# Kernel tuning notes

Measured on AMD Instinct MI355X. Metric: run time of the kernel, lower is better.

The kernel has to match this reference:

```python
import jax, jax.numpy as jnp
import numpy as np

N = 30000       # num atoms (all examples concatenated)
E = 480000      # total num edges (avg degree 16)
H = 128         # hidden_channels
R = 50          # num_rbf
NB = 3          # num interaction blocks
NEX = 64        # num examples (molecules)
NTYPES = 100    # atom type vocabulary
CUT = 10.0      # cutoff_upper


def setup_inputs() -> dict:
    key = jax.random.key(0)
    ks = jax.random.split(key, 20)
    s = 0.05
    inp = {
        "pos": jax.random.uniform(ks[0], (N, 3), dtype=jnp.float32) * 10.0,
        "atom_types": jax.random.randint(ks[1], (N,), 0, NTYPES),
        "edge_index": jax.random.randint(ks[2], (2, E), 0, N),
        "batch": jnp.sort(jax.random.randint(ks[3], (N,), 0, NEX)),
        # learned parameters
        "embedding": jax.random.normal(ks[4], (NTYPES, H), dtype=jnp.float32) * s,
        "filt_w1": jax.random.normal(ks[5], (NB, R, H), dtype=jnp.float32) * s,
        "filt_b1": jnp.zeros((NB, H), jnp.float32),
        "filt_w2": jax.random.normal(ks[6], (NB, H, H), dtype=jnp.float32) * s,
        "filt_b2": jnp.zeros((NB, H), jnp.float32),
        "lin1_w": jax.random.normal(ks[7], (NB, H, H), dtype=jnp.float32) * s,  # no bias
        "lin2_w": jax.random.normal(ks[8], (NB, H, H), dtype=jnp.float32) * s,
        "lin2_b": jnp.zeros((NB, H), jnp.float32),
        "blk_w": jax.random.normal(ks[9], (NB, H, H), dtype=jnp.float32) * s,
        "blk_b": jnp.zeros((NB, H), jnp.float32),
        "out_w1": jax.random.normal(ks[10], (H, H // 2), dtype=jnp.float32) * s,
        "out_b1": jnp.zeros((H // 2,), jnp.float32),
        "out_w2": jax.random.normal(ks[11], (H // 2, 1), dtype=jnp.float32) * s,
        "out_b2": jnp.zeros((1,), jnp.float32),
    }
    return inp


def reference(pos, atom_types, edge_index, batch, embedding,
              filt_w1, filt_b1, filt_w2, filt_b2,
              lin1_w, lin2_w, lin2_b, blk_w, blk_b,
              out_w1, out_b1, out_w2, out_b2):
    src, dst = edge_index[0], edge_index[1]
    # pairwise distances along edges
    diff = pos[src] - pos[dst]                        # [E,3]
    d = jnp.sqrt(jnp.sum(diff * diff, axis=-1) + 1e-12)  # [E]
    # Gaussian RBF expansion (PyG GaussianSmearing)
    offset = jnp.linspace(0.0, CUT, R, dtype=jnp.float32)
    coeff = -0.5 / (offset[1] - offset[0]) ** 2
    rbf = jnp.exp(coeff * (d[:, None] - offset) ** 2)  # [E,R]
    # cosine cutoff envelope
    C = 0.5 * (jnp.cos(d * jnp.pi / CUT) + 1.0) * (d < CUT)  # [E]

    x = embedding[atom_types]                         # [N,H]
    for b in range(NB):
        # filter network: Linear -> Tanh -> Linear, modulated by cutoff
        W = jnp.tanh(rbf @ filt_w1[b] + filt_b1[b]) @ filt_w2[b] + filt_b2[b]
        W = W * C[:, None]                            # [E,H]
        # cfconv: lin1 (no bias), gather-multiply-scatter, lin2
        h = x @ lin1_w[b]                             # [N,H]
        msg = h[src] * W                              # [E,H]
        agg = jax.ops.segment_sum(msg, dst, num_segments=N)  # [N,H]
        h = agg @ lin2_w[b] + lin2_b[b]
        # interaction block: activation + linear, residual update
        x = x + (jnp.tanh(h) @ blk_w[b] + blk_b[b])
    # output network: per-atom energy then scatter-sum per molecule
    e = jnp.tanh(x @ out_w1 + out_b1) @ out_w2 + out_b2     # [N,1]
    energy = jax.ops.segment_sum(e, batch, num_segments=NEX)  # [NEX,1]
    return energy.reshape(-1)
```

## Files before the change

kernel.cpp:

```cpp
#include <hip/hip_runtime.h>

typedef unsigned short ushort_t;
typedef _Float16 half8 __attribute__((ext_vector_type(8)));
typedef float f32x4 __attribute__((ext_vector_type(4)));

constexpr int NN  = 30000;
constexpr int EE  = 480000;
constexpr int NEXM = 64;
constexpr int ATB = 16;
constexpr int NSB = (NN + 255) / 256;
constexpr int NBINS = 2048;
constexpr int TROWS = 2064;

#define MFMA16(a,b,c) __builtin_amdgcn_mfma_f32_16x16x32_f16((a),(b),(c),0,0,0)
#define LDS_ADD(p,v) __hip_atomic_fetch_add((p),(v),__ATOMIC_RELAXED,__HIP_MEMORY_SCOPE_WORKGROUP)
#define LGKM_WAIT asm volatile("s_waitcnt lgkmcnt(0)" ::: "memory")

__device__ __forceinline__ float fast_tanh(float x){
  float e2 = __builtin_amdgcn_exp2f(x * 2.885390081777927f);
  return 1.f - 2.f * __builtin_amdgcn_rcpf(e2 + 1.f);
}
__device__ __forceinline__ ushort_t f2h(float v){
  union { _Float16 h; ushort_t s; } cv; cv.h = (_Float16)v; return cv.s;
}

__global__ __launch_bounds__(256) void prep_weights(
  const float* __restrict__ fw1, const float* __restrict__ fb1,
  const float* __restrict__ fw2, const float* __restrict__ l1w,
  const float* __restrict__ l2w, const float* __restrict__ bw,
  const float* __restrict__ ow1, ushort_t* __restrict__ frags)
{
  int u = blockIdx.x*256 + threadIdx.x;
  float val;
  if (u < 24576){
    int b = u >> 13; int v = u & 8191;
    int j = v & 7, lane = (v>>3)&63, fid = v>>9;
    int mt = fid>>1, ks = fid&1;
    int f1 = mt*16 + (lane&15);
    int k  = ks*32 + ((lane>>4)&3)*8 + j;
    val = (k < 50) ? fw1[(b*50 + k)*128 + f1] : (k == 50 ? fb1[b*128 + f1] : 0.f);
  } else if (u < 73728){
    int v = u - 24576; int b = v >> 14; int v2 = v & 16383;
    int j = v2&7, lane = (v2>>3)&63, fid = v2>>9;
    int mt = fid>>2, ks = fid&3;
    int n = mt*16 + (lane&15);
    int k = ks*32 + ((lane>>4)&3)*8 + j;
    val = fw2[b*16384 + k*128 + n];
  } else if (u < 221184){
    int v = u - 73728; int g = v / 49152; int v1 = v - g*49152;
    int b = v1 >> 14; int v2 = v1 & 16383;
    int j = v2&7, lane=(v2>>3)&63, fid=v2>>9;
    int mt = fid>>2, ks = fid&3;
    int n = mt*16 + (lane&15);
    int k = ks*32 + ((lane>>4)&3)*8 + j;
    const float* W = (g==0? l2w : (g==1? bw : l1w));
    val = W[b*16384 + k*128 + n];
  } else {
    int v2 = u - 221184;
    int j = v2&7, lane=(v2>>3)&63, fid=v2>>9;
    int mt = fid>>2, ks = fid&3;
    int n = mt*16 + (lane&15);
    int k = ks*32 + ((lane>>4)&3)*8 + j;
    val = ow1[k*64 + n];
  }
  frags[u] = f2h(val);
}

__global__ __launch_bounds__(256) void count_k(
  const int* __restrict__ ei, int* __restrict__ cnt)
{
  int e = blockIdx.x*256 + threadIdx.x;
  atomicAdd(cnt + ei[EE + e], 1);
}

__global__ __launch_bounds__(256) void scan1(
  const int* __restrict__ cnt, int* __restrict__ seg, int* __restrict__ bsum)
{
  __shared__ int ws[4];
  int i = blockIdx.x*256 + threadIdx.x;
  int lane = threadIdx.x & 63, w = threadIdx.x >> 6;
  int v = (i < NN) ? cnt[i] : 0;
  int s = v;
  #pragma unroll
  for (int o=1;o<64;o<<=1){ int t = __shfl_up(s,o,64); if (lane>=o) s += t; }
  if (lane == 63) ws[w] = s;
  __syncthreads();
  int add = 0;
  #pragma unroll
  for (int j=0;j<3;j++) if (w > j) add += ws[j];
  s += add;
  if (i < NN) seg[i] = s - v;
  if (threadIdx.x == 255) bsum[blockIdx.x] = s;
}

__global__ __launch_bounds__(128) void scan2(int* __restrict__ bsum)
{
  __shared__ int w0tot;
  int tid = threadIdx.x, lane = tid & 63, w = tid >> 6;
  int v = (tid < NSB) ? bsum[tid] : 0;
  int s = v;
  #pragma unroll
  for (int o=1;o<64;o<<=1){ int t = __shfl_up(s,o,64); if (lane>=o) s += t; }
  if (w == 0 && lane == 63) w0tot = s;
  __syncthreads();
  if (w == 1) s += w0tot;
  if (tid < NSB) bsum[tid] = s - v;
}

__global__ __launch_bounds__(256) void scan3(
  int* __restrict__ seg, const int* __restrict__ bsum)
{
  int i = blockIdx.x*256 + threadIdx.x;
  if (i < NN) seg[i] += bsum[blockIdx.x];
}

__global__ __launch_bounds__(256) void scatter_meta(
  const float* __restrict__ pos, const int* __restrict__ ei,
  int* __restrict__ off, uint2* __restrict__ meta2)
{
  int e = blockIdx.x*256 + threadIdx.x;
  int s = ei[e], d = ei[EE + e];
  float dx = pos[s*3+0]-pos[d*3+0];
  float dy = pos[s*3+1]-pos[d*3+1];
  float dz = pos[s*3+2]-pos[d*3+2];
  float dist = sqrtf(dx*dx+dy*dy+dz*dz + 1e-12f);
  float t = fminf(dist, 10.f) * ((float)NBINS / 10.f);
  int p = atomicAdd(off + d, 1);
  uint2 m;
  m.x = __float_as_uint(t);
  m.y = (unsigned)s;
  meta2[p] = m;
}

__global__ __launch_bounds__(256) void build_table(
  const ushort_t* __restrict__ w1a, const ushort_t* __restrict__ w2a,
  const float* __restrict__ fb2, ushort_t* __restrict__ tab)
{
  __shared__ ushort_t st[4*2112];
  const int wave = threadIdx.x>>6, lane = threadIdx.x&63;
  const int quad = lane>>4, n15 = lane&15;
  const int b = blockIdx.x / 33, tg = blockIdx.x % 33;
  const int tile = tg*4 + wave;
  if (tile >= TROWS/16) return;
  const half8* w1v = (const half8*)(w1a + b*8192);
  const half8* w2v = (const half8*)(w2a + b*16384);
  ushort_t* tw = st + wave*2112;
  half8 a1[16];
  #pragma unroll
  for (int i=0;i<16;i++) a1[i] = w1v[i*64 + lane];
  f32x4 b2v[8];
  #pragma unroll
  for (int mt=0;mt<8;mt++) b2v[mt] = *(const f32x4*)(fb2 + b*128 + mt*16 + quad*4);
  const f32x4 zero4 = {0.f,0.f,0.f,0.f};
  const float dd = 10.f/49.f;
  const float coefl2 = (-0.5f/(dd*dd)) * 1.4426950408889634f;
  const float dbin = 10.f/(float)NBINS;

  float de = (float)(tile*16 + n15) * dbin;
  float Cv = (de < 10.f) ? 0.5f*(cosf(de*0.31415926535897931f)+1.f) : 0.f;
  half8 rb0, rb1;
  #pragma unroll
  for (int j=0;j<8;j++){
    int k0 = quad*8 + j;
    float t0 = de - (float)k0*dd;
    rb0[j] = (_Float16)__builtin_amdgcn_exp2f(coefl2*t0*t0);
    int k1 = 32 + quad*8 + j;
    float v1;
    if (k1 < 50){ float t1 = de - (float)k1*dd; v1 = __builtin_amdgcn_exp2f(coefl2*t1*t1); }
    else v1 = (k1 == 50) ? 1.f : 0.f;
    rb1[j] = (_Float16)v1;
  }
  f32x4 acc1[8];
  #pragma unroll
  for (int mt=0;mt<8;mt++){
    acc1[mt] = MFMA16(a1[mt*2],   rb0, zero4);
    acc1[mt] = MFMA16(a1[mt*2+1], rb1, acc1[mt]);
  }
  #pragma unroll
  for (int mt=0;mt<8;mt++){
    union { ushort_t s[4]; uint2 v; } pk;
    #pragma unroll
    for (int r=0;r<4;r++) pk.s[r] = f2h(fast_tanh(acc1[mt][r]));
    *(uint2*)(tw + n15*132 + mt*16 + quad*4) = pk.v;
  }
  LGKM_WAIT;
  f32x4 acc2[8];
  #pragma unroll
  for (int mt=0;mt<8;mt++) acc2[mt] = zero4;
  #pragma unroll
  for (int ks=0;ks<4;ks++){
    const ushort_t* ra = tw + n15*132 + ks*32 + quad*8;
    union { uint2 v[2]; half8 h16; } cc;
    cc.v[0] = *(const uint2*)(ra);
    cc.v[1] = *(const uint2*)(ra + 4);
    half8 tb = cc.h16;
    #pragma unroll
    for (int mt=0;mt<8;mt++) acc2[mt] = MFMA16(w2v[(mt*4+ks)*64 + lane], tb, acc2[mt]);
  }
  LGKM_WAIT;
  #pragma unroll
  for (int mt=0;mt<8;mt++){
    f32x4 v = acc2[mt] + b2v[mt];
    union { ushort_t s[4]; uint2 q; } pk;
    #pragma unroll
    for (int r=0;r<4;r++) pk.s[r] = f2h(v[r] * Cv);
    *(uint2*)(tw + n15*132 + mt*16 + quad*4) = pk.q;
  }
  LGKM_WAIT;
  ushort_t* dstb = tab + ((size_t)b*TROWS + tile*16)*128;
  #pragma unroll
  for (int it=0;it<4;it++){
    int off = it*512 + lane*8;
    uint4 v = *(const uint4*)(tw + (off>>7)*132 + (off&127));
    *(uint4*)(dstb + (size_t)(off>>7)*128 + (off&127)) = v;
  }
}

__global__ __launch_bounds__(256) void embed_h0(
  const int* __restrict__ atype, const float* __restrict__ emb,
  const ushort_t* __restrict__ l1T, float* __restrict__ x, ushort_t* __restrict__ h)
{
  __shared__ float xbuf[4*2112];
  const int wave = threadIdx.x>>6, lane = threadIdx.x&63;
  const int quad = lane>>4, n15 = lane&15;
  float* xw = xbuf + wave*2112;
  ushort_t* sw = (ushort_t*)xw;
  const half8* wv = (const half8*)l1T;
  const f32x4 zero4 = {0.f,0.f,0.f,0.f};
  const int ntiles = NN/16;
  const int stride = gridDim.x*4;
  for (int tile = blockIdx.x*4 + wave; tile < ntiles; tile += stride){
    int a0 = tile*16;
    int typ = atype[a0 + n15];
    const f32x4* av = (const f32x4*)(emb + (size_t)typ*128);
    half8 bg[4]; f32x4 xl[4], xh[4];
    #pragma unroll
    for (int ks=0;ks<4;ks++){
      f32x4 lo = av[ks*8 + quad*2];
      f32x4 hi = av[ks*8 + quad*2 + 1];
      xl[ks] = lo; xh[ks] = hi;
      half8 bh;
      #pragma unroll
      for (int i=0;i<4;i++){ bh[i]=(_Float16)lo[i]; bh[4+i]=(_Float16)hi[i]; }
      bg[ks] = bh;
    }
    f32x4 acc[8];
    #pragma unroll
    for (int mt=0;mt<8;mt++) acc[mt] = zero4;
    #pragma unroll
    for (int ks=0;ks<4;ks++){
      #pragma unroll
      for (int mt=0;mt<8;mt++) acc[mt] = MFMA16(wv[(mt*4+ks)*64 + lane], bg[ks], acc[mt]);
    }
    #pragma unroll
    for (int ks=0;ks<4;ks++){
      *(f32x4*)(xw + n15*132 + ks*32 + quad*8)     = xl[ks];
      *(f32x4*)(xw + n15*132 + ks*32 + quad*8 + 4) = xh[ks];
    }
    LGKM_WAIT;
    {
      float* gx = x + (size_t)a0*128;
      #pragma unroll
      for (int it=0;it<8;it++){
        int off = it*256 + lane*4;
        f32x4 v = *(const f32x4*)(xw + (off>>7)*132 + (off&127));
        *(f32x4*)(gx + off) = v;
      }
    }
    LGKM_WAIT;
    #pragma unroll
    for (int mt=0;mt<8;mt++){
      union { ushort_t s[4]; uint2 v; } pk;
      #pragma unroll
      for (int r=0;r<4;r++) pk.s[r] = f2h(acc[mt][r]);
      *(uint2*)(sw + n15*132 + mt*16 + quad*4) = pk.v;
    }
    LGKM_WAIT;
    {
      ushort_t* gh = h + (size_t)a0*128;
      #pragma unroll
      for (int it=0;it<4;it++){
        int off = it*512 + lane*8;
        uint4 v = *(const uint4*)(sw + (off>>7)*132 + (off&127));
        *(uint4*)(gh + off) = v;
      }
    }
    LGKM_WAIT;
  }
}

__global__ __launch_bounds__(256,6) void mega_pass(
  const uint2* __restrict__ meta2, const ushort_t* __restrict__ hin,
  ushort_t* __restrict__ hout, const ushort_t* __restrict__ tab,
  const ushort_t* __restrict__ l2T, const ushort_t* __restrict__ bkT,
  const ushort_t* __restrict__ l1Tn,
  const float* __restrict__ l2b, const float* __restrict__ bb,
  const int* __restrict__ segend, float* __restrict__ x, int do_h)
{
  __shared__ ushort_t nt[2112];
  const int wave = threadIdx.x>>6, lane = threadIdx.x&63;
  const int quad = lane>>4, n15 = lane&15;
  const int base = blockIdx.x*ATB;
  const f32x4 zero4 = {0.f,0.f,0.f,0.f};

  const int cg = threadIdx.x >> 4, ctf = threadIdx.x & 15;
  const int ca = base + cg;
  const int clo = (ca==0) ? 0 : segend[ca-1];
  const int chi = segend[ca];
  float acc[8];
  #pragma unroll
  for (int j=0;j<8;j++) acc[j] = 0.f;

  if (clo < chi){
    uint2 me = *(const uint2*)(meta2 + clo);
    float t = __uint_as_float(me.x);
    int i0 = (int)t;
    float fr = t - (float)i0;
    const half8* tp = (const half8*)(tab + (size_t)i0*128) + ctf;
    half8 w0 = tp[0];
    half8 w1 = tp[16];
    half8 hv = *(const half8*)(hin + (size_t)me.y*128 + ctf*8);
    int e = clo;
    while (true){
      int en = e + 1;
      bool more = en < chi;
      half8 w0n = w0, w1n = w1, hvn = hv; float frn = fr;
      if (more){
        uint2 m2 = *(const uint2*)(meta2 + en);
        float t2 = __uint_as_float(m2.x);
        int i2 = (int)t2;
        frn = t2 - (float)i2;
        const half8* tpn = (const half8*)(tab + (size_t)i2*128) + ctf;
        w0n = tpn[0];
        w1n = tpn[16];
        hvn = *(const half8*)(hin + (size_t)m2.y*128 + ctf*8);
      }
      #pragma unroll
      for (int j=0;j<8;j++){
        float wl = (float)w0[j] + fr * ((float)w1[j] - (float)w0[j]);
        acc[j] += wl * (float)hv[j];
      }
      if (!more) break;
      w0 = w0n; w1 = w1n; hv = hvn; fr = frn; e = en;
    }
  }

  {
    union { ushort_t s[8]; uint4 q; } pk;
    #pragma unroll
    for (int j=0;j<8;j++) pk.s[j] = f2h(acc[j]);
    *(uint4*)(nt + cg*132 + ctf*8) = pk.q;
  }
  __syncthreads();

  {
    half8 bg[4];
    #pragma unroll
    for (int ks=0;ks<4;ks++){
      const ushort_t* ra = nt + n15*132 + ks*32 + quad*8;
      union { uint2 v[2]; half8 h16; } cc;
      cc.v[0] = *(const uint2*)(ra);
      cc.v[1] = *(const uint2*)(ra + 4);
      bg[ks] = cc.h16;
    }
    __syncthreads();
    const half8* wAv = (const half8*)l2T;
    f32x4 accA[2];
    #pragma unroll
    for (int i=0;i<2;i++) accA[i] = zero4;
    #pragma unroll
    for (int ks=0;ks<4;ks++){
      #pragma unroll
      for (int i=0;i<2;i++)
        accA[i] = MFMA16(wAv[((wave*2+i)*4+ks)*64 + lane], bg[ks], accA[i]);
    }
    #pragma unroll
    for (int i=0;i<2;i++){
      int mt = wave*2 + i;
      f32x4 bv = *(const f32x4*)(l2b + mt*16 + quad*4);
      union { ushort_t s[4]; uint2 v; } pk;
      #pragma unroll
      for (int r=0;r<4;r++) pk.s[r] = f2h(fast_tanh(accA[i][r] + bv[r]));
      *(uint2*)(nt + n15*132 + mt*16 + quad*4) = pk.v;
    }
    __syncthreads();
    half8 bg2[4];
    #pragma unroll
    for (int ks=0;ks<4;ks++){
      const ushort_t* ra = nt + n15*132 + ks*32 + quad*8;
      union { uint2 v[2]; half8 h16; } cc;
      cc.v[0] = *(const uint2*)(ra);
      cc.v[1] = *(const uint2*)(ra + 4);
      bg2[ks] = cc.h16;
    }
    __syncthreads();
    const half8* wBv = (const half8*)bkT;
    f32x4 accB[2];
    #pragma unroll
    for (int i=0;i<2;i++) accB[i] = zero4;
    #pragma unroll
    for (int ks=0;ks<4;ks++){
      #pragma unroll
      for (int i=0;i<2;i++)
        accB[i] = MFMA16(wBv[((wave*2+i)*4+ks)*64 + lane], bg2[ks], accB[i]);
    }
    f32x4 xn[2];
    float* xp = x + (size_t)(base + n15)*128;
    #pragma unroll
    for (int i=0;i<2;i++){
      int mt = wave*2 + i;
      f32x4 bv = *(const f32x4*)(bb + mt*16 + quad*4);
      f32x4 xv = *(const f32x4*)(xp + mt*16 + quad*4);
      xn[i] = xv + accB[i] + bv;
      *(f32x4*)(xp + mt*16 + quad*4) = xn[i];
    }
    if (do_h){
      #pragma unroll
      for (int i=0;i<2;i++){
        int mt = wave*2 + i;
        union { ushort_t s[4]; uint2 v; } pk;
        #pragma unroll
        for (int r=0;r<4;r++) pk.s[r] = f2h(xn[i][r]);
        *(uint2*)(nt + n15*132 + mt*16 + quad*4) = pk.v;
      }
      __syncthreads();
      half8 bg3[4];
      #pragma unroll
      for (int ks=0;ks<4;ks++){
        const ushort_t* ra = nt + n15*132 + ks*32 + quad*8;
        union { uint2 v[2]; half8 h16; } cc;
        cc.v[0] = *(const uint2*)(ra);
        cc.v[1] = *(const uint2*)(ra + 4);
        bg3[ks] = cc.h16;
      }
      const half8* wCv = (const half8*)l1Tn;
      f32x4 accC[2];
      #pragma unroll
      for (int i=0;i<2;i++) accC[i] = zero4;
      #pragma unroll
      for (int ks=0;ks<4;ks++){
        #pragma unroll
        for (int i=0;i<2;i++)
          accC[i] = MFMA16(wCv[((wave*2+i)*4+ks)*64 + lane], bg3[ks], accC[i]);
      }
      ushort_t* hp = hout + (size_t)(base + n15)*128;
      #pragma unroll
      for (int i=0;i<2;i++){
        int mt = wave*2 + i;
        union { ushort_t s[4]; uint2 v; } pk;
        #pragma unroll
        for (int r=0;r<4;r++) pk.s[r] = f2h(accC[i][r]);
        *(uint2*)(hp + mt*16 + quad*4) = pk.v;
      }
    }
  }
}

__global__ __launch_bounds__(256) void out_head(
  const float* __restrict__ x, const ushort_t* __restrict__ o1T,
  const float* __restrict__ ob1, const float* __restrict__ ow2,
  const float* __restrict__ ob2, const int* __restrict__ batch,
  float* __restrict__ out)
{
  __shared__ float part[NEXM];
  const int tid = threadIdx.x;
  if (tid < NEXM) part[tid] = 0.f;
  __syncthreads();
  const int wave = tid>>6, lane = tid&63;
  const int quad = lane>>4, n15 = lane&15;
  const half8* wv = (const half8*)o1T;
  const f32x4 zero4 = {0.f,0.f,0.f,0.f};
  f32x4 ow2v[4], ob1v[4];
  #pragma unroll
  for (int mt=0;mt<4;mt++){
    ow2v[mt] = *(const f32x4*)(ow2 + mt*16 + quad*4);
    ob1v[mt] = *(const f32x4*)(ob1 + mt*16 + quad*4);
  }
  const float ob2v = ob2[0];
  const int ntiles = NN/16;
  const int stride = gridDim.x*4;
  for (int tile = blockIdx.x*4 + wave; tile < ntiles; tile += stride){
    int a0 = tile*16;
    half8 bg[4];
    const f32x4* av = (const f32x4*)(x + (size_t)(a0 + n15)*128);
    #pragma unroll
    for (int ks=0;ks<4;ks++){
      f32x4 lo = av[ks*8 + quad*2];
      f32x4 hi = av[ks*8 + quad*2 + 1];
      half8 bh;
      #pragma unroll
      for (int i=0;i<4;i++){ bh[i]=(_Float16)lo[i]; bh[4+i]=(_Float16)hi[i]; }
      bg[ks] = bh;
    }
    f32x4 acc[4];
    #pragma unroll
    for (int mt=0;mt<4;mt++) acc[mt] = zero4;
    #pragma unroll
    for (int ks=0;ks<4;ks++){
      #pragma unroll
      for (int mt=0;mt<4;mt++) acc[mt] = MFMA16(wv[(mt*4+ks)*64 + lane], bg[ks], acc[mt]);
    }
    float e = 0.f;
    #pragma unroll
    for (int mt=0;mt<4;mt++){
      f32x4 v = acc[mt] + ob1v[mt];
      #pragma unroll
      for (int r=0;r<4;r++) e += fast_tanh(v[r]) * ow2v[mt][r];
    }
    e += __shfl_xor(e, 16, 64);
    e += __shfl_xor(e, 32, 64);
    if (quad == 0){
      int a = a0 + n15;
      LDS_ADD(&part[batch[a]], e + ob2v);
    }
  }
  __syncthreads();
  if (tid < NEXM)
    __hip_atomic_fetch_add(out + tid, part[tid], __ATOMIC_RELAXED, __HIP_MEMORY_SCOPE_AGENT);
}

extern "C" void kernel_launch(void* const* d_in, const int* in_sizes, int n_in,
                              void* d_out, int out_size, void* d_ws, size_t ws_size,
                              hipStream_t stream)
{
  const float* pos  = (const float*)d_in[0];
  const int*   atyp = (const int*)  d_in[1];
  const int*   ei   = (const int*)  d_in[2];
  const int*   bat  = (const int*)  d_in[3];
  const float* emb  = (const float*)d_in[4];
  const float* fw1  = (const float*)d_in[5];
  const float* fb1  = (const float*)d_in[6];
  const float* fw2  = (const float*)d_in[7];
  const float* fb2  = (const float*)d_in[8];
  const float* l1w  = (const float*)d_in[9];
  const float* l2w  = (const float*)d_in[10];
  const float* l2b  = (const float*)d_in[11];
  const float* bw   = (const float*)d_in[12];
  const float* bb   = (const float*)d_in[13];
  const float* ow1  = (const float*)d_in[14];
  const float* ob1  = (const float*)d_in[15];
  const float* ow2  = (const float*)d_in[16];
  const float* ob2  = (const float*)d_in[17];
  float* out = (float*)d_out;

  char* p = (char*)d_ws;
  uint2*    meta2 = (uint2*)p;   p += (size_t)EE*8;
  ushort_t* hA   = (ushort_t*)p; p += (size_t)NN*128*2;
  ushort_t* hB   = (ushort_t*)p; p += (size_t)NN*128*2;
  float*    x    = (float*)p;    p += (size_t)NN*128*4;
  ushort_t* frags = (ushort_t*)p; p += 229376*2;
  int*      segend = (int*)p;    p += (size_t)NN*4;
  int*      bsum  = (int*)p;     p += 512;
  ushort_t* tab  = (ushort_t*)p; p += (size_t)3*TROWS*128*2;

  int* cnt = (int*)x;

  ushort_t* w1T = frags;
  ushort_t* w2T = frags + 24576;
  ushort_t* l2T = frags + 73728;
  ushort_t* bkT = frags + 122880;
  ushort_t* l1T = frags + 172032;
  ushort_t* o1T = frags + 221184;

  hipMemsetAsync(d_out, 0, NEXM*sizeof(float), stream);
  hipMemsetAsync(cnt, 0, NN*sizeof(int), stream);
  prep_weights<<<896,256,0,stream>>>(fw1,fb1,fw2,l1w,l2w,bw,ow1,frags);
  build_table<<<99,256,0,stream>>>(w1T, w2T, fb2, tab);
  count_k<<<EE/256,256,0,stream>>>(ei, cnt);
  scan1<<<NSB,256,0,stream>>>(cnt, segend, bsum);
  scan2<<<1,128,0,stream>>>(bsum);
  scan3<<<NSB,256,0,stream>>>(segend, bsum);
  scatter_meta<<<EE/256,256,0,stream>>>(pos, ei, segend, meta2);
  embed_h0<<<512,256,0,stream>>>(atyp, emb, l1T, x, hA);

  for (int b=0;b<3;b++){
    const ushort_t* hin = (b & 1) ? hB : hA;
    ushort_t*       hoB = (b & 1) ? hA : hB;
    int do_h = (b < 2) ? 1 : 0;
    mega_pass<<<NN/ATB,256,0,stream>>>(meta2, hin, hoB,
                                       tab + (size_t)b*TROWS*128,
                                       l2T + b*16384, bkT + b*16384,
                                       l1T + ((b<2)?(b+1):0)*16384,
                                       l2b + b*128, bb + b*128,
                                       segend, x, do_h);
  }
  out_head<<<256,256,0,stream>>>(x, o1T, ob1, ow2, ob2, bat, out);
}
```

Measured before the change: 305.1 us.

## Interleave filter table rows with deltas and deepen gather prefetch pipeline

Adds a pair_table kernel that stores each filter-table row next to its delta to the following row. Each edge's interpolation then reads one contiguous 32-byte chunk per lane instead of two rows 256 bytes apart, and saves a subtraction. The per-edge gather loop now keeps two edges of data in flight and prefetches metadata up to four edges ahead, to hide gather latency. In exchange it adds an extra kernel launch, doubles the table footprint, and uses more registers in a kernel launched with an occupancy bound of 6.

New measurement: 314.5 us. +3.1%, slower.

```diff
diff --git a/kernel.cpp b/kernel.cpp
--- a/kernel.cpp
+++ b/kernel.cpp
@@ -207,13 +207,29 @@
     *(uint2*)(tw + n15*132 + mt*16 + quad*4) = pk.q;
   }
   LGKM_WAIT;
-  ushort_t* dstb = tab + ((size_t)b*TROWS + tile*16)*128;
+  ushort_t* dstb = tab + ((size_t)tile*16)*128 + (size_t)b*TROWS*128;
   #pragma unroll
   for (int it=0;it<4;it++){
     int off = it*512 + lane*8;
     uint4 v = *(const uint4*)(tw + (off>>7)*132 + (off&127));
     *(uint4*)(dstb + (size_t)(off>>7)*128 + (off&127)) = v;
   }
+}
+
+__global__ __launch_bounds__(256) void pair_table(
+  const ushort_t* __restrict__ tab, ushort_t* __restrict__ tabP)
+{
+  int u = blockIdx.x*256 + threadIdx.x;
+  if (u >= 3*2063*16) return;
+  int b = u / (2063*16); int v = u - b*(2063*16);
+  int i = v >> 4, c = v & 15;
+  const ushort_t* rb = tab + (size_t)b*TROWS*128;
+  half8 r0 = *(const half8*)(rb + (size_t)i*128 + c*8);
+  half8 r1 = *(const half8*)(rb + (size_t)(i+1)*128 + c*8);
+  half8 dl = r1 - r0;
+  ushort_t* dst = tabP + (size_t)b*TROWS*256 + (size_t)i*256 + c*16;
+  *(half8*)dst = r0;
+  *(half8*)(dst+8) = dl;
 }
 
 __global__ __launch_bounds__(256) void embed_h0(
@@ -291,7 +307,7 @@
 
 __global__ __launch_bounds__(256,6) void mega_pass(
   const uint2* __restrict__ meta2, const ushort_t* __restrict__ hin,
-  ushort_t* __restrict__ hout, const ushort_t* __restrict__ tab,
+  ushort_t* __restrict__ hout, const ushort_t* __restrict__ tabP,
   const ushort_t* __restrict__ l2T, const ushort_t* __restrict__ bkT,
   const ushort_t* __restrict__ l1Tn,
   const float* __restrict__ l2b, const float* __restrict__ bb,
@@ -312,36 +328,53 @@
   for (int j=0;j<8;j++) acc[j] = 0.f;
 
   if (clo < chi){
-    uint2 me = *(const uint2*)(meta2 + clo);
-    float t = __uint_as_float(me.x);
-    int i0 = (int)t;
-    float fr = t - (float)i0;
-    const half8* tp = (const half8*)(tab + (size_t)i0*128) + ctf;
-    half8 w0 = tp[0];
-    half8 w1 = tp[16];
-    half8 hv = *(const half8*)(hin + (size_t)me.y*128 + ctf*8);
-    int e = clo;
-    while (true){
-      int en = e + 1;
-      bool more = en < chi;
-      half8 w0n = w0, w1n = w1, hvn = hv; float frn = fr;
-      if (more){
-        uint2 m2 = *(const uint2*)(meta2 + en);
-        float t2 = __uint_as_float(m2.x);
-        int i2 = (int)t2;
-        frn = t2 - (float)i2;
-        const half8* tpn = (const half8*)(tab + (size_t)i2*128) + ctf;
-        w0n = tpn[0];
-        w1n = tpn[16];
-        hvn = *(const half8*)(hin + (size_t)m2.y*128 + ctf*8);
-      }
-      #pragma unroll
-      for (int j=0;j<8;j++){
-        float wl = (float)w0[j] + fr * ((float)w1[j] - (float)w0[j]);
-        acc[j] += wl * (float)hv[j];
-      }
-      if (!more) break;
-      w0 = w0n; w1 = w1n; hv = hvn; fr = frn; e = en;
+    const int last = chi - 1;
+    const ushort_t* tbc  = tabP + ctf*16;
+    const ushort_t* hinc = hin + ctf*8;
+    uint2 mA = meta2[clo];
+    uint2 mB = meta2[(clo+1 <= last) ? clo+1 : last];
+    uint2 mC = meta2[(clo+2 <= last) ? clo+2 : last];
+    uint2 mD = meta2[(clo+3 <= last) ? clo+3 : last];
+    float frA, frB;
+    half8 w0A, dlA, hvA, w0B, dlB, hvB;
+    {
+      float t = __uint_as_float(mA.x); int i0 = (int)t; frA = t - (float)i0;
+      const ushort_t* tp = tbc + (size_t)i0*256;
+      w0A = *(const half8*)tp; dlA = *(const half8*)(tp + 8);
+      hvA = *(const half8*)(hinc + (size_t)mA.y*128);
+    }
+    {
+      float t = __uint_as_float(mB.x); int i0 = (int)t; frB = t - (float)i0;
+      const ushort_t* tp = tbc + (size_t)i0*256;
+      w0B = *(const half8*)tp; dlB = *(const half8*)(tp + 8);
+      hvB = *(const half8*)(hinc + (size_t)mB.y*128);
+    }
+    for (int e = clo; ; ){
+      #pragma unroll
+      for (int j=0;j<8;j++)
+        acc[j] += ((float)w0A[j] + frA * (float)dlA[j]) * (float)hvA[j];
+      if (e+1 > last) break;
+      {
+        float t = __uint_as_float(mC.x); int i0 = (int)t; frA = t - (float)i0;
+        const ushort_t* tp = tbc + (size_t)i0*256;
+        w0A = *(const half8*)tp; dlA = *(const half8*)(tp + 8);
+        hvA = *(const half8*)(hinc + (size_t)mC.y*128);
+        int e4 = e + 4;
+        mC = meta2[(e4 <= last) ? e4 : last];
+      }
+      #pragma unroll
+      for (int j=0;j<8;j++)
+        acc[j] += ((float)w0B[j] + frB * (float)dlB[j]) * (float)hvB[j];
+      if (e+2 > last) break;
+      {
+        float t = __uint_as_float(mD.x); int i0 = (int)t; frB = t - (float)i0;
+        const ushort_t* tp = tbc + (size_t)i0*256;
+        w0B = *(const half8*)tp; dlB = *(const half8*)(tp + 8);
+        hvB = *(const half8*)(hinc + (size_t)mD.y*128);
+        int e5 = e + 5;
+        mD = meta2[(e5 <= last) ? e5 : last];
+      }
+      e += 2;
     }
   }
 
@@ -552,6 +585,7 @@
   int*      segend = (int*)p;    p += (size_t)NN*4;
   int*      bsum  = (int*)p;     p += 512;
   ushort_t* tab  = (ushort_t*)p; p += (size_t)3*TROWS*128*2;
+  ushort_t* tabP = (ushort_t*)p; p += (size_t)3*TROWS*256*2;
 
   int* cnt = (int*)x;
 
@@ -566,6 +600,7 @@
   hipMemsetAsync(cnt, 0, NN*sizeof(int), stream);
   prep_weights<<<896,256,0,stream>>>(fw1,fb1,fw2,l1w,l2w,bw,ow1,frags);
   build_table<<<99,256,0,stream>>>(w1T, w2T, fb2, tab);
+  pair_table<<<387,256,0,stream>>>(tab, tabP);
   count_k<<<EE/256,256,0,stream>>>(ei, cnt);
   scan1<<<NSB,256,0,stream>>>(cnt, segend, bsum);
   scan2<<<1,128,0,stream>>>(bsum);
@@ -578,7 +613,7 @@
     ushort_t*       hoB = (b & 1) ? hA : hB;
     int do_h = (b < 2) ? 1 : 0;
     mega_pass<<<NN/ATB,256,0,stream>>>(meta2, hin, hoB,
-                                       tab + (size_t)b*TROWS*128,
+                                       tabP + (size_t)b*TROWS*256,
                                        l2T + b*16384, bkT + b*16384,
                                        l1T + ((b<2)?(b+1):0)*16384,
                                        l2b + b*128, bb + b*128,
```

## Fuse independent preprocessing kernels and fold output head into last interaction pass

Applied to the files above, without the earlier changes.

Merges prep_weights with count_k, build_table with scan1, and scatter_meta with embed_h0 into single launches using block-index ranges, removing several kernel launches and the output memset. The output MLP and per-molecule reduction move into the final mega_pass, which skips writing x back and does global atomics per atom instead of per-block LDS reductions. Launch bounds for mega_pass change to 8 waves per SIMD hint, which may increase register pressure/spilling. Out zeroing in fused_prep relies on ordering before the last mega_pass.

Result: slower. 461.0 us (+51.1%).

```diff
diff --git a/kernel.cpp b/kernel.cpp
--- a/kernel.cpp
+++ b/kernel.cpp
@@ -24,73 +24,159 @@
   union { _Float16 h; ushort_t s; } cv; cv.h = (_Float16)v; return cv.s;
 }
 
-__global__ __launch_bounds__(256) void prep_weights(
+__global__ __launch_bounds__(256) void fused_prep(
   const float* __restrict__ fw1, const float* __restrict__ fb1,
   const float* __restrict__ fw2, const float* __restrict__ l1w,
   const float* __restrict__ l2w, const float* __restrict__ bw,
-  const float* __restrict__ ow1, ushort_t* __restrict__ frags)
-{
-  int u = blockIdx.x*256 + threadIdx.x;
-  float val;
-  if (u < 24576){
-    int b = u >> 13; int v = u & 8191;
-    int j = v & 7, lane = (v>>3)&63, fid = v>>9;
-    int mt = fid>>1, ks = fid&1;
-    int f1 = mt*16 + (lane&15);
-    int k  = ks*32 + ((lane>>4)&3)*8 + j;
-    val = (k < 50) ? fw1[(b*50 + k)*128 + f1] : (k == 50 ? fb1[b*128 + f1] : 0.f);
-  } else if (u < 73728){
-    int v = u - 24576; int b = v >> 14; int v2 = v & 16383;
-    int j = v2&7, lane = (v2>>3)&63, fid = v2>>9;
-    int mt = fid>>2, ks = fid&3;
-    int n = mt*16 + (lane&15);
-    int k = ks*32 + ((lane>>4)&3)*8 + j;
-    val = fw2[b*16384 + k*128 + n];
-  } else if (u < 221184){
-    int v = u - 73728; int g = v / 49152; int v1 = v - g*49152;
-    int b = v1 >> 14; int v2 = v1 & 16383;
-    int j = v2&7, lane=(v2>>3)&63, fid=v2>>9;
-    int mt = fid>>2, ks = fid&3;
-    int n = mt*16 + (lane&15);
-    int k = ks*32 + ((lane>>4)&3)*8 + j;
-    const float* W = (g==0? l2w : (g==1? bw : l1w));
-    val = W[b*16384 + k*128 + n];
+  const float* __restrict__ ow1, ushort_t* __restrict__ frags,
+  const int* __restrict__ ei, int* __restrict__ cnt, float* __restrict__ out)
+{
+  const int bid = blockIdx.x;
+  if (bid < 896){
+    if (bid == 0 && threadIdx.x < NEXM) out[threadIdx.x] = 0.f;
+    int u = bid*256 + threadIdx.x;
+    float val;
+    if (u < 24576){
+      int b = u >> 13; int v = u & 8191;
+      int j = v & 7, lane = (v>>3)&63, fid = v>>9;
+      int mt = fid>>1, ks = fid&1;
+      int f1 = mt*16 + (lane&15);
+      int k  = ks*32 + ((lane>>4)&3)*8 + j;
+      val = (k < 50) ? fw1[(b*50 + k)*128 + f1] : (k == 50 ? fb1[b*128 + f1] : 0.f);
+    } else if (u < 73728){
+      int v = u - 24576; int b = v >> 14; int v2 = v & 16383;
+      int j = v2&7, lane = (v2>>3)&63, fid = v2>>9;
+      int mt = fid>>2, ks = fid&3;
+      int n = mt*16 + (lane&15);
+      int k = ks*32 + ((lane>>4)&3)*8 + j;
+      val = fw2[b*16384 + k*128 + n];
+    } else if (u < 221184){
+      int v = u - 73728; int g = v / 49152; int v1 = v - g*49152;
+      int b = v1 >> 14; int v2 = v1 & 16383;
+      int j = v2&7, lane=(v2>>3)&63, fid=v2>>9;
+      int mt = fid>>2, ks = fid&3;
+      int n = mt*16 + (lane&15);
+      int k = ks*32 + ((lane>>4)&3)*8 + j;
+      const float* W = (g==0? l2w : (g==1? bw : l1w));
+      val = W[b*16384 + k*128 + n];
+    } else {
+      int v2 = u - 221184;
+      int j = v2&7, lane=(v2>>3)&63, fid=v2>>9;
+      int mt = fid>>2, ks = fid&3;
+      int n = mt*16 + (lane&15);
+      int k = ks*32 + ((lane>>4)&3)*8 + j;
+      val = ow1[k*64 + n];
+    }
+    frags[u] = f2h(val);
   } else {
-    int v2 = u - 221184;
-    int j = v2&7, lane=(v2>>3)&63, fid=v2>>9;
-    int mt = fid>>2, ks = fid&3;
-    int n = mt*16 + (lane&15);
-    int k = ks*32 + ((lane>>4)&3)*8 + j;
-    val = ow1[k*64 + n];
-  }
-  frags[u] = f2h(val);
-}
-
-__global__ __launch_bounds__(256) void count_k(
-  const int* __restrict__ ei, int* __restrict__ cnt)
-{
-  int e = blockIdx.x*256 + threadIdx.x;
-  atomicAdd(cnt + ei[EE + e], 1);
-}
-
-__global__ __launch_bounds__(256) void scan1(
+    int e = (bid-896)*256 + threadIdx.x;
+    atomicAdd(cnt + ei[EE + e], 1);
+  }
+}
+
+__global__ __launch_bounds__(256) void fused_mid(
+  const ushort_t* __restrict__ w1a, const ushort_t* __restrict__ w2a,
+  const float* __restrict__ fb2, ushort_t* __restrict__ tab,
   const int* __restrict__ cnt, int* __restrict__ seg, int* __restrict__ bsum)
 {
-  __shared__ int ws[4];
-  int i = blockIdx.x*256 + threadIdx.x;
-  int lane = threadIdx.x & 63, w = threadIdx.x >> 6;
-  int v = (i < NN) ? cnt[i] : 0;
-  int s = v;
-  #pragma unroll
-  for (int o=1;o<64;o<<=1){ int t = __shfl_up(s,o,64); if (lane>=o) s += t; }
-  if (lane == 63) ws[w] = s;
-  __syncthreads();
-  int add = 0;
-  #pragma unroll
-  for (int j=0;j<3;j++) if (w > j) add += ws[j];
-  s += add;
-  if (i < NN) seg[i] = s - v;
-  if (threadIdx.x == 255) bsum[blockIdx.x] = s;
+  __shared__ ushort_t st[4*2112];
+  const int bid = blockIdx.x;
+  if (bid < 99){
+    const int wave = threadIdx.x>>6, lane = threadIdx.x&63;
+    const int quad = lane>>4, n15 = lane&15;
+    const int b = bid / 33, tg = bid % 33;
+    const int tile = tg*4 + wave;
+    if (tile >= TROWS/16) return;
+    const half8* w1v = (const half8*)(w1a + b*8192);
+    const half8* w2v = (const half8*)(w2a + b*16384);
+    ushort_t* tw = st + wave*2112;
+    half8 a1[16];
+    #pragma unroll
+    for (int i=0;i<16;i++) a1[i] = w1v[i*64 + lane];
+    f32x4 b2v[8];
+    #pragma unroll
+    for (int mt=0;mt<8;mt++) b2v[mt] = *(const f32x4*)(fb2 + b*128 + mt*16 + quad*4);
+    const f32x4 zero4 = {0.f,0.f,0.f,0.f};
+    const float dd = 10.f/49.f;
+    const float coefl2 = (-0.5f/(dd*dd)) * 1.4426950408889634f;
+    const float dbin = 10.f/(float)NBINS;
+
+    float de = (float)(tile*16 + n15) * dbin;
+    float Cv = (de < 10.f) ? 0.5f*(cosf(de*0.31415926535897931f)+1.f) : 0.f;
+    half8 rb0, rb1;
+    #pragma unroll
+    for (int j=0;j<8;j++){
+      int k0 = quad*8 + j;
+      float t0 = de - (float)k0*dd;
+      rb0[j] = (_Float16)__builtin_amdgcn_exp2f(coefl2*t0*t0);
+      int k1 = 32 + quad*8 + j;
+      float v1;
+      if (k1 < 50){ float t1 = de - (float)k1*dd; v1 = __builtin_amdgcn_exp2f(coefl2*t1*t1); }
+      else v1 = (k1 == 50) ? 1.f : 0.f;
+      rb1[j] = (_Float16)v1;
+    }
+    f32x4 acc1[8];
+    #pragma unroll
+    for (int mt=0;mt<8;mt++){
+      acc1[mt] = MFMA16(a1[mt*2],   rb0, zero4);
+      acc1[mt] = MFMA16(a1[mt*2+1], rb1, acc1[mt]);
+    }
+    #pragma unroll
+    for (int mt=0;mt<8;mt++){
+      union { ushort_t s[4]; uint2 v; } pk;
+      #pragma unroll
+      for (int r=0;r<4;r++) pk.s[r] = f2h(fast_tanh(acc1[mt][r]));
+      *(uint2*)(tw + n15*132 + mt*16 + quad*4) = pk.v;
+    }
+    LGKM_WAIT;
+    f32x4 acc2[8];
+    #pragma unroll
+    for (int mt=0;mt<8;mt++) acc2[mt] = zero4;
+    #pragma unroll
+    for (int ks=0;ks<4;ks++){
+      const ushort_t* ra = tw + n15*132 + ks*32 + quad*8;
+      union { uint2 v[2]; half8 h16; } cc;
+      cc.v[0] = *(const uint2*)(ra);
+      cc.v[1] = *(const uint2*)(ra + 4);
+      half8 tb = cc.h16;
+      #pragma unroll
+      for (int mt=0;mt<8;mt++) acc2[mt] = MFMA16(w2v[(mt*4+ks)*64 + lane], tb, acc2[mt]);
+    }
+    LGKM_WAIT;
+    #pragma unroll
+    for (int mt=0;mt<8;mt++){
+      f32x4 v = acc2[mt] + b2v[mt];
+      union { ushort_t s[4]; uint2 q; } pk;
+      #pragma unroll
+      for (int r=0;r<4;r++) pk.s[r] = f2h(v[r] * Cv);
+      *(uint2*)(tw + n15*132 + mt*16 + quad*4) = pk.q;
+    }
+    LGKM_WAIT;
+    ushort_t* dstb = tab + ((size_t)tile*16)*128 + (size_t)b*TROWS*128;
+    #pragma unroll
+    for (int it=0;it<4;it++){
+      int off = it*512 + lane*8;
+      uint4 v = *(const uint4*)(tw + (off>>7)*132 + (off&127));
+      *(uint4*)(dstb + (size_t)(off>>7)*128 + (off&127)) = v;
+    }
+  } else {
+    int* ws = (int*)st;
+    const int sb = bid - 99;
+    int i = sb*256 + threadIdx.x;
+    int lane = threadIdx.x & 63, w = threadIdx.x >> 6;
+    int v = (i < NN) ? cnt[i] : 0;
+    int s = v;
+    #pragma unroll
+    for (int o=1;o<64;o<<=1){ int t = __shfl_up(s,o,64); if (lane>=o) s += t; }
+    if (lane == 63) ws[w] = s;
+    __syncthreads();
+    int add = 0;
+    #pragma unroll
+    for (int j=0;j<3;j++) if (w > j) add += ws[j];
+    s += add;
+    if (i < NN) seg[i] = s - v;
+    if (threadIdx.x == 255) bsum[sb] = s;
+  }
 }
 
 __global__ __launch_bounds__(128) void scan2(int* __restrict__ bsum)
@@ -114,113 +200,30 @@
   if (i < NN) seg[i] += bsum[blockIdx.x];
 }
 
-__global__ __launch_bounds__(256) void scatter_meta(
+__global__ __launch_bounds__(256) void fused_tail(
   const float* __restrict__ pos, const int* __restrict__ ei,
-  int* __restrict__ off, uint2* __restrict__ meta2)
-{
-  int e = blockIdx.x*256 + threadIdx.x;
-  int s = ei[e], d = ei[EE + e];
-  float dx = pos[s*3+0]-pos[d*3+0];
-  float dy = pos[s*3+1]-pos[d*3+1];
-  float dz = pos[s*3+2]-pos[d*3+2];
-  float dist = sqrtf(dx*dx+dy*dy+dz*dz + 1e-12f);
-  float t = fminf(dist, 10.f) * ((float)NBINS / 10.f);
-  int p = atomicAdd(off + d, 1);
-  uint2 m;
-  m.x = __float_as_uint(t);
-  m.y = (unsigned)s;
-  meta2[p] = m;
-}
-
-__global__ __launch_bounds__(256) void build_table(
-  const ushort_t* __restrict__ w1a, const ushort_t* __restrict__ w2a,
-  const float* __restrict__ fb2, ushort_t* __restrict__ tab)
-{
-  __shared__ ushort_t st[4*2112];
-  const int wave = threadIdx.x>>6, lane = threadIdx.x&63;
-  const int quad = lane>>4, n15 = lane&15;
-  const int b = blockIdx.x / 33, tg = blockIdx.x % 33;
-  const int tile = tg*4 + wave;
-  if (tile >= TROWS/16) return;
-  const half8* w1v = (const half8*)(w1a + b*8192);
-  const half8* w2v = (const half8*)(w2a + b*16384);
-  ushort_t* tw = st + wave*2112;
-  half8 a1[16];
-  #pragma unroll
-  for (int i=0;i<16;i++) a1[i] = w1v[i*64 + lane];
-  f32x4 b2v[8];
-  #pragma unroll
-  for (int mt=0;mt<8;mt++) b2v[mt] = *(const f32x4*)(fb2 + b*128 + mt*16 + quad*4);
-  const f32x4 zero4 = {0.f,0.f,0.f,0.f};
-  const float dd = 10.f/49.f;
-  const float coefl2 = (-0.5f/(dd*dd)) * 1.4426950408889634f;
-  const float dbin = 10.f/(float)NBINS;
-
-  float de = (float)(tile*16 + n15) * dbin;
-  float Cv = (de < 10.f) ? 0.5f*(cosf(de*0.31415926535897931f)+1.f) : 0.f;
-  half8 rb0, rb1;
-  #pragma unroll
-  for (int j=0;j<8;j++){
-    int k0 = quad*8 + j;
-    float t0 = de - (float)k0*dd;
-    rb0[j] = (_Float16)__builtin_amdgcn_exp2f(coefl2*t0*t0);
-    int k1 = 32 + quad*8 + j;
-    float v1;
-    if (k1 < 50){ float t1 = de - (float)k1*dd; v1 = __builtin_amdgcn_exp2f(coefl2*t1*t1); }
-    else v1 = (k1 == 50) ? 1.f : 0.f;
-    rb1[j] = (_Float16)v1;
-  }
-  f32x4 acc1[8];
-  #pragma unroll
-  for (int mt=0;mt<8;mt++){
-    acc1[mt] = MFMA16(a1[mt*2],   rb0, zero4);
-    acc1[mt] = MFMA16(a1[mt*2+1], rb1, acc1[mt]);
-  }
-  #pragma unroll
-  for (int mt=0;mt<8;mt++){
-    union { ushort_t s[4]; uint2 v; } pk;
-    #pragma unroll
-    for (int r=0;r<4;r++) pk.s[r] = f2h(fast_tanh(acc1[mt][r]));
-    *(uint2*)(tw + n15*132 + mt*16 + quad*4) = pk.v;
-  }
-  LGKM_WAIT;
-  f32x4 acc2[8];
-  #pragma unroll
-  for (int mt=0;mt<8;mt++) acc2[mt] = zero4;
-  #pragma unroll
-  for (int ks=0;ks<4;ks++){
-    const ushort_t* ra = tw + n15*132 + ks*32 + quad*8;
-    union { uint2 v[2]; half8 h16; } cc;
-    cc.v[0] = *(const uint2*)(ra);
-    cc.v[1] = *(const uint2*)(ra + 4);
-    half8 tb = cc.h16;
-    #pragma unroll
-    for (int mt=0;mt<8;mt++) acc2[mt] = MFMA16(w2v[(mt*4+ks)*64 + lane], tb, acc2[mt]);
-  }
-  LGKM_WAIT;
-  #pragma unroll
-  for (int mt=0;mt<8;mt++){
-    f32x4 v = acc2[mt] + b2v[mt];
-    union { ushort_t s[4]; uint2 q; } pk;
-    #pragma unroll
-    for (int r=0;r<4;r++) pk.s[r] = f2h(v[r] * Cv);
-    *(uint2*)(tw + n15*132 + mt*16 + quad*4) = pk.q;
-  }
-  LGKM_WAIT;
-  ushort_t* dstb = tab + ((size_t)b*TROWS + tile*16)*128;
-  #pragma unroll
-  for (int it=0;it<4;it++){
-    int off = it*512 + lane*8;
-    uint4 v = *(const uint4*)(tw + (off>>7)*132 + (off&127));
-    *(uint4*)(dstb + (size_t)(off>>7)*128 + (off&127)) = v;
-  }
-}
-
-__global__ __launch_bounds__(256) void embed_h0(
+  int* __restrict__ off, uint2* __restrict__ meta2,
   const int* __restrict__ atype, const float* __restrict__ emb,
   const ushort_t* __restrict__ l1T, float* __restrict__ x, ushort_t* __restrict__ h)
 {
   __shared__ float xbuf[4*2112];
+  const int bid = blockIdx.x;
+  if (bid < 1875){
+    int e = bid*256 + threadIdx.x;
+    int s = ei[e], d = ei[EE + e];
+    float dx = pos[s*3+0]-pos[d*3+0];
+    float dy = pos[s*3+1]-pos[d*3+1];
+    float dz = pos[s*3+2]-pos[d*3+2];
+    float dist = sqrtf(dx*dx+dy*dy+dz*dz + 1e-12f);
+    float t = fminf(dist, 10.f) * ((float)NBINS / 10.f);
+    int p = atomicAdd(off + d, 1);
+    uint2 m;
+    m.x = __float_as_uint(t);
+    m.y = (unsigned)s;
+    meta2[p] = m;
+    return;
+  }
+  const int vb = bid - 1875;
   const int wave = threadIdx.x>>6, lane = threadIdx.x&63;
   const int quad = lane>>4, n15 = lane&15;
   float* xw = xbuf + wave*2112;
@@ -228,8 +231,8 @@
   const half8* wv = (const half8*)l1T;
   const f32x4 zero4 = {0.f,0.f,0.f,0.f};
   const int ntiles = NN/16;
-  const int stride = gridDim.x*4;
-  for (int tile = blockIdx.x*4 + wave; tile < ntiles; tile += stride){
+  const int stride = 512*4;
+  for (int tile = vb*4 + wave; tile < ntiles; tile += stride){
     int a0 = tile*16;
     int typ = atype[a0 + n15];
     const f32x4* av = (const f32x4*)(emb + (size_t)typ*128);
@@ -262,9 +265,9 @@
       float* gx = x + (size_t)a0*128;
       #pragma unroll
       for (int it=0;it<8;it++){
-        int off = it*256 + lane*4;
-        f32x4 v = *(const f32x4*)(xw + (off>>7)*132 + (off&127));
-        *(f32x4*)(gx + off) = v;
+        int off2 = it*256 + lane*4;
+        f32x4 v = *(const f32x4*)(xw + (off2>>7)*132 + (off2&127));
+        *(f32x4*)(gx + off2) = v;
       }
     }
     LGKM_WAIT;
@@ -280,22 +283,25 @@
       ushort_t* gh = h + (size_t)a0*128;
       #pragma unroll
       for (int it=0;it<4;it++){
-        int off = it*512 + lane*8;
-        uint4 v = *(const uint4*)(sw + (off>>7)*132 + (off&127));
-        *(uint4*)(gh + off) = v;
-      }
-    }
-    LGKM_WAIT;
-  }
-}
-
-__global__ __launch_bounds__(256,6) void mega_pass(
+        int off2 = it*512 + lane*8;
+        uint4 v = *(const uint4*)(sw + (off2>>7)*132 + (off2&127));
+        *(uint4*)(gh + off2) = v;
+      }
+    }
+    LGKM_WAIT;
+  }
+}
+
+__global__ __launch_bounds__(256,8) void mega_pass(
   const uint2* __restrict__ meta2, const ushort_t* __restrict__ hin,
   ushort_t* __restrict__ hout, const ushort_t* __restrict__ tab,
   const ushort_t* __restrict__ l2T, const ushort_t* __restrict__ bkT,
-  const ushort_t* __restrict__ l1Tn,
+  const ushort_t* __restrict__ l1Tn, const ushort_t* __restrict__ o1T,
   const float* __restrict__ l2b, const float* __restrict__ bb,
-  const int* __restrict__ segend, float* __restrict__ x, int do_h)
+  const float* __restrict__ ob1, const float* __restrict__ ow2,
+  const float* __restrict__ ob2, const int* __restrict__ batch,
+  float* __restrict__ out,
+  const int* __restrict__ segend, float* __restrict__ x, int do_h, int last)
 {
   __shared__ ushort_t nt[2112];
   const int wave = threadIdx.x>>6, lane = threadIdx.x&63;
@@ -412,7 +418,7 @@
       f32x4 bv = *(const f32x4*)(bb + mt*16 + quad*4);
       f32x4 xv = *(const f32x4*)(xp + mt*16 + quad*4);
       xn[i] = xv + accB[i] + bv;
-      *(f32x4*)(xp + mt*16 + quad*4) = xn[i];
+      if (!last) *(f32x4*)(xp + mt*16 + quad*4) = xn[i];
     }
     if (do_h){
       #pragma unroll
@@ -452,71 +458,54 @@
         for (int r=0;r<4;r++) pk.s[r] = f2h(accC[i][r]);
         *(uint2*)(hp + mt*16 + quad*4) = pk.v;
       }
-    }
-  }
-}
-
-__global__ __launch_bounds__(256) void out_head(
-  const float* __restrict__ x, const ushort_t* __restrict__ o1T,
-  const float* __restrict__ ob1, const float* __restrict__ ow2,
-  const float* __restrict__ ob2, const int* __restrict__ batch,
-  float* __restrict__ out)
-{
-  __shared__ float part[NEXM];
-  const int tid = threadIdx.x;
-  if (tid < NEXM) part[tid] = 0.f;
-  __syncthreads();
-  const int wave = tid>>6, lane = tid&63;
-  const int quad = lane>>4, n15 = lane&15;
-  const half8* wv = (const half8*)o1T;
-  const f32x4 zero4 = {0.f,0.f,0.f,0.f};
-  f32x4 ow2v[4], ob1v[4];
-  #pragma unroll
-  for (int mt=0;mt<4;mt++){
-    ow2v[mt] = *(const f32x4*)(ow2 + mt*16 + quad*4);
-    ob1v[mt] = *(const f32x4*)(ob1 + mt*16 + quad*4);
-  }
-  const float ob2v = ob2[0];
-  const int ntiles = NN/16;
-  const int stride = gridDim.x*4;
-  for (int tile = blockIdx.x*4 + wave; tile < ntiles; tile += stride){
-    int a0 = tile*16;
-    half8 bg[4];
-    const f32x4* av = (const f32x4*)(x + (size_t)(a0 + n15)*128);
-    #pragma unroll
-    for (int ks=0;ks<4;ks++){
-      f32x4 lo = av[ks*8 + quad*2];
-      f32x4 hi = av[ks*8 + quad*2 + 1];
-      half8 bh;
-      #pragma unroll
-      for (int i=0;i<4;i++){ bh[i]=(_Float16)lo[i]; bh[4+i]=(_Float16)hi[i]; }
-      bg[ks] = bh;
-    }
-    f32x4 acc[4];
-    #pragma unroll
-    for (int mt=0;mt<4;mt++) acc[mt] = zero4;
-    #pragma unroll
-    for (int ks=0;ks<4;ks++){
-      #pragma unroll
-      for (int mt=0;mt<4;mt++) acc[mt] = MFMA16(wv[(mt*4+ks)*64 + lane], bg[ks], acc[mt]);
-    }
-    float e = 0.f;
-    #pragma unroll
-    for (int mt=0;mt<4;mt++){
-      f32x4 v = acc[mt] + ob1v[mt];
-      #pragma unroll
-      for (int r=0;r<4;r++) e += fast_tanh(v[r]) * ow2v[mt][r];
-    }
-    e += __shfl_xor(e, 16, 64);
-    e += __shfl_xor(e, 32, 64);
-    if (quad == 0){
-      int a = a0 + n15;
-      LDS_ADD(&part[batch[a]], e + ob2v);
-    }
-  }
-  __syncthreads();
-  if (tid < NEXM)
-    __hip_atomic_fetch_add(out + tid, part[tid], __ATOMIC_RELAXED, __HIP_MEMORY_SCOPE_AGENT);
+    } else if (last){
+      #pragma unroll
+      for (int i=0;i<2;i++){
+        int mt = wave*2 + i;
+        union { ushort_t s[4]; uint2 v; } pk;
+        #pragma unroll
+        for (int r=0;r<4;r++) pk.s[r] = f2h(xn[i][r]);
+        *(uint2*)(nt + n15*132 + mt*16 + quad*4) = pk.v;
+      }
+      __syncthreads();
+      if (wave == 0){
+        half8 bg3[4];
+        #pragma unroll
+        for (int ks=0;ks<4;ks++){
+          const ushort_t* ra = nt + n15*132 + ks*32 + quad*8;
+          union { uint2 v[2]; half8 h16; } cc;
+          cc.v[0] = *(const uint2*)(ra);
+          cc.v[1] = *(const uint2*)(ra + 4);
+          bg3[ks] = cc.h16;
+        }
+        const half8* wv = (const half8*)o1T;
+        f32x4 acco[4];
+        #pragma unroll
+        for (int mt=0;mt<4;mt++) acco[mt] = zero4;
+        #pragma unroll
+        for (int ks=0;ks<4;ks++){
+          #pragma unroll
+          for (int mt=0;mt<4;mt++) acco[mt] = MFMA16(wv[(mt*4+ks)*64 + lane], bg3[ks], acco[mt]);
+        }
+        float e = 0.f;
+        #pragma unroll
+        for (int mt=0;mt<4;mt++){
+          f32x4 bv = *(const f32x4*)(ob1 + mt*16 + quad*4);
+          f32x4 wo = *(const f32x4*)(ow2 + mt*16 + quad*4);
+          f32x4 v = acco[mt] + bv;
+          #pragma unroll
+          for (int r=0;r<4;r++) e += fast_tanh(v[r]) * wo[r];
+        }
+        e += __shfl_xor(e, 16, 64);
+        e += __shfl_xor(e, 32, 64);
+        if (quad == 0){
+          int a = base + n15;
+          __hip_atomic_fetch_add(out + batch[a], e + ob2[0],
+                                 __ATOMIC_RELAXED, __HIP_MEMORY_SCOPE_AGENT);
+        }
+      }
+    }
+  }
 }
 
 extern "C" void kernel_launch(void* const* d_in, const int* in_sizes, int n_in,
@@ -562,27 +551,25 @@
   ushort_t* l1T = frags + 172032;
   ushort_t* o1T = frags + 221184;
 
-  hipMemsetAsync(d_out, 0, NEXM*sizeof(float), stream);
   hipMemsetAsync(cnt, 0, NN*sizeof(int), stream);
-  prep_weights<<<896,256,0,stream>>>(fw1,fb1,fw2,l1w,l2w,bw,ow1,frags);
-  build_table<<<99,256,0,stream>>>(w1T, w2T, fb2, tab);
-  count_k<<<EE/256,256,0,stream>>>(ei, cnt);
-  scan1<<<NSB,256,0,stream>>>(cnt, segend, bsum);
+  fused_prep<<<896+1875,256,0,stream>>>(fw1,fb1,fw2,l1w,l2w,bw,ow1,frags,ei,cnt,out);
+  fused_mid<<<99+NSB,256,0,stream>>>(w1T, w2T, fb2, tab, cnt, segend, bsum);
   scan2<<<1,128,0,stream>>>(bsum);
   scan3<<<NSB,256,0,stream>>>(segend, bsum);
-  scatter_meta<<<EE/256,256,0,stream>>>(pos, ei, segend, meta2);
-  embed_h0<<<512,256,0,stream>>>(atyp, emb, l1T, x, hA);
+  fused_tail<<<1875+512,256,0,stream>>>(pos, ei, segend, meta2,
+                                        atyp, emb, l1T, x, hA);
 
   for (int b=0;b<3;b++){
     const ushort_t* hin = (b & 1) ? hB : hA;
     ushort_t*       hoB = (b & 1) ? hA : hB;
     int do_h = (b < 2) ? 1 : 0;
+    int last = (b == 2) ? 1 : 0;
     mega_pass<<<NN/ATB,256,0,stream>>>(meta2, hin, hoB,
                                        tab + (size_t)b*TROWS*128,
                                        l2T + b*16384, bkT + b*16384,
-                                       l1T + ((b<2)?(b+1):0)*16384,
+                                       l1T + ((b<2)?(b+1):0)*16384, o1T,
                                        l2b + b*128, bb + b*128,
-                                       segend, x, do_h);
-  }
-  out_head<<<256,256,0,stream>>>(x, o1T, ob1, ow2, ob2, bat, out);
-}
+                                       ob1, ow2, ob2, bat, out,
+                                       segend, x, do_h, last);
+  }
+}
```
